# Kernel optimization log

Measured on AMD Instinct MI355X. Metric: run time of the kernel, lower is better.

Reference implementation:

```python
import jax, jax.numpy as jnp
import numpy as np

TOP_K = 8  # config['n_experts_per_token']


def setup_inputs() -> dict:
    key = jax.random.key(0)
    k1, k2 = jax.random.split(key)
    d_hidden, n_experts, n_tokens = 4096, 64, 32768
    x = jax.random.normal(k1, (n_tokens, d_hidden), dtype=jnp.float32)
    # nn.Linear weight, shape [num_experts, d_hidden], kaiming-ish scale
    W_g = jax.random.normal(k2, (n_experts, d_hidden), dtype=jnp.float32) / np.sqrt(d_hidden)
    return {"x": x, "W_g": W_g}


def reference(x, W_g):
    # logits = x @ W_g^T : [n_tokens, n_experts]
    logits = jnp.einsum('td,ed->te', x, W_g)
    scores = jax.nn.softmax(logits, axis=-1)
    # torch.topk(sorted=False) returns the same value/index set; lax.top_k is sorted
    vals, idx = jax.lax.top_k(scores, TOP_K)
    return vals, idx
```

## Files before the change

### kernel.cpp

```cpp
#include <hip/hip_runtime.h>
#include <hip/hip_fp16.h>


typedef _Float16 half8 __attribute__((ext_vector_type(8)));
typedef float floatx4 __attribute__((ext_vector_type(4)));

constexpr int D = 4096;
constexpr int NE = 64;
constexpr int MBLK = 64;
constexpr int BK = 64;
constexpr int KCHUNKS = D / BK;

__device__ __forceinline__ void split8(float4 p, float4 q, float sc, half8& h, half8& l) {
    float f[8] = {p.x, p.y, p.z, p.w, q.x, q.y, q.z, q.w};
#pragma unroll
    for (int i = 0; i < 8; ++i) {
        float v = f[i] * sc;
        _Float16 hi = (_Float16)v;
        h[i] = hi;
        l[i] = (_Float16)(v - (float)hi);
    }
}

__global__ __launch_bounds__(256, 2) void moe_gate_kernel(
    const float* __restrict__ x, const float* __restrict__ wg,
    float* __restrict__ out_vals, float* __restrict__ out_idx,
    int* __restrict__ flag_ws, int cap)
{
    __shared__ alignas(16) _Float16 Xh[MBLK * BK];
    __shared__ alignas(16) _Float16 Xl[MBLK * BK];
    __shared__ alignas(16) _Float16 Wh[NE * BK];
    __shared__ alignas(16) _Float16 Wl[NE * BK];

    const int tid  = (int)threadIdx.x;
    const int lane = tid & 63;
    const int wv   = tid >> 6;
    const int tb   = (int)blockIdx.x * MBLK;

    const int s0 = tid, s1 = tid + 256;
    const int t0 = s0 >> 3, k80 = s0 & 7;
    const int t1 = s1 >> 3, k81 = s1 & 7;

    const float* xp0 = x  + (size_t)(tb + t0) * D + k80 * 8;
    const float* xp1 = x  + (size_t)(tb + t1) * D + k81 * 8;
    const float* wp0 = wg + (size_t)t0 * D + k80 * 8;
    const float* wp1 = wg + (size_t)t1 * D + k81 * 8;

    const int xo0 = (((t0 >> 4) * 2 + (k80 >> 2)) * 64 + (k80 & 3) * 16 + (t0 & 15)) * 8;
    const int xo1 = (((t1 >> 4) * 2 + (k81 >> 2)) * 64 + (k81 & 3) * 16 + (t1 & 15)) * 8;

    float4 ra0, ra1, rb0, rb1, rc0, rc1, rd0, rd1;
#define LOADCHUNK(kc) do { const int off_ = (kc) * BK;                        \
        ra0 = *(const float4*)(xp0 + off_); ra1 = *(const float4*)(xp0 + off_ + 4); \
        rb0 = *(const float4*)(xp1 + off_); rb1 = *(const float4*)(xp1 + off_ + 4); \
        rc0 = *(const float4*)(wp0 + off_); rc1 = *(const float4*)(wp0 + off_ + 4); \
        rd0 = *(const float4*)(wp1 + off_); rd1 = *(const float4*)(wp1 + off_ + 4); } while (0)

    floatx4 acc[4] = {{0,0,0,0},{0,0,0,0},{0,0,0,0},{0,0,0,0}};

    LOADCHUNK(0);
    for (int kc = 0; kc < KCHUNKS; ++kc) {
        half8 hx0, lx0, hx1, lx1, hw0, lw0, hw1, lw1;
        split8(ra0, ra1, 1.0f,  hx0, lx0);
        split8(rb0, rb1, 1.0f,  hx1, lx1);
        split8(rc0, rc1, 64.0f, hw0, lw0);
        split8(rd0, rd1, 64.0f, hw1, lw1);
        if (kc) __syncthreads();
        *(half8*)(Xh + xo0) = hx0; *(half8*)(Xl + xo0) = lx0;
        *(half8*)(Xh + xo1) = hx1; *(half8*)(Xl + xo1) = lx1;
        *(half8*)(Wh + xo0) = hw0; *(half8*)(Wl + xo0) = lw0;
        *(half8*)(Wh + xo1) = hw1; *(half8*)(Wl + xo1) = lw1;
        if (kc + 1 < KCHUNKS) LOADCHUNK(kc + 1);
        __syncthreads();
#pragma unroll
        for (int ks = 0; ks < 2; ++ks) {
            const half8 ah = *(const half8*)(Xh + ((wv * 2 + ks) * 64 + lane) * 8);
            const half8 al = *(const half8*)(Xl + ((wv * 2 + ks) * 64 + lane) * 8);
#pragma unroll
            for (int nt = 0; nt < 4; ++nt) {
                const half8 bh = *(const half8*)(Wh + ((nt * 2 + ks) * 64 + lane) * 8);
                const half8 bl = *(const half8*)(Wl + ((nt * 2 + ks) * 64 + lane) * 8);
                acc[nt] = __builtin_amdgcn_mfma_f32_16x16x32_f16(ah, bh, acc[nt], 0, 0, 0);
                acc[nt] = __builtin_amdgcn_mfma_f32_16x16x32_f16(al, bh, acc[nt], 0, 0, 0);
                acc[nt] = __builtin_amdgcn_mfma_f32_16x16x32_f16(ah, bl, acc[nt], 0, 0, 0);
            }
        }
    }
#undef LOADCHUNK

    const int g = lane >> 4, c = lane & 15;
    const float inv64 = 0.015625f;
#pragma unroll
    for (int r = 0; r < 4; ++r) {
        float s[4];
#pragma unroll
        for (int nt = 0; nt < 4; ++nt) s[nt] = acc[nt][r] * inv64;
        float m = fmaxf(fmaxf(s[0], s[1]), fmaxf(s[2], s[3]));
#pragma unroll
        for (int off = 1; off < 16; off <<= 1) m = fmaxf(m, __shfl_xor(m, off));
        float p[4]; float t = 0.0f;
#pragma unroll
        for (int nt = 0; nt < 4; ++nt) { p[nt] = expf(s[nt] - m); t += p[nt]; }
#pragma unroll
        for (int off = 1; off < 16; off <<= 1) t += __shfl_xor(t, off);
        const float inv = 1.0f / t;
#pragma unroll
        for (int nt = 0; nt < 4; ++nt) p[nt] *= inv;

        const int tok = tb + wv * 16 + g * 4 + r;
        float prev = 0.0f;
        bool flagged = false;
#pragma unroll
        for (int i = 0; i < 9; ++i) {
            float bv = p[0]; int bn = 0;
            if (p[1] > bv) { bv = p[1]; bn = 1; }
            if (p[2] > bv) { bv = p[2]; bn = 2; }
            if (p[3] > bv) { bv = p[3]; bn = 3; }
            int be = bn * 16 + c;
#pragma unroll
            for (int off = 1; off < 16; off <<= 1) {
                float ov = __shfl_xor(bv, off);
                int   oe = __shfl_xor(be, off);
                if (ov > bv || (ov == bv && oe < be)) { bv = ov; be = oe; }
            }
            if (i > 0 && (prev - bv) < prev * 5e-5f) flagged = true;
            prev = bv;
            if (i < 8 && c == i) {
                out_vals[(size_t)tok * 8 + i] = bv;
                out_idx [(size_t)tok * 8 + i] = (float)be;
            }
            if (c == (be & 15)) p[be >> 4] = -1.0f;
        }
        if (flagged && c == 0 && cap > 0) {
            int pos = atomicAdd(flag_ws, 1);
            if (pos < cap) flag_ws[4 + pos] = tok;
        }
    }
}

__global__ __launch_bounds__(256) void moe_refine_kernel(
    const float* __restrict__ x, const float* __restrict__ wg,
    float* __restrict__ out_vals, float* __restrict__ out_idx,
    const int* __restrict__ flag_ws, int cap)
{
    const int count = min(flag_ws[0], cap);
    const int* list = flag_ws + 4;
    __shared__ double part[256];
    for (int it = (int)blockIdx.x; it < count; it += (int)gridDim.x) {
        const int tok = list[it];
        const int e = (int)threadIdx.x & 63, ch = (int)threadIdx.x >> 6;
        const float4* xr = (const float4*)(x + (size_t)tok * D + ch * 1024);
        const float4* wr = (const float4*)(wg + (size_t)e * D + ch * 1024);
        double s0 = 0, s1 = 0, s2 = 0, s3 = 0;
#pragma unroll 4
        for (int k = 0; k < 256; ++k) {
            float4 a = xr[k], b = wr[k];
            s0 += (double)a.x * (double)b.x; s1 += (double)a.y * (double)b.y;
            s2 += (double)a.z * (double)b.z; s3 += (double)a.w * (double)b.w;
        }
        part[threadIdx.x] = (s0 + s1) + (s2 + s3);
        __syncthreads();
        if (threadIdx.x < 64) {
            double l = part[e] + part[e + 64] + part[e + 128] + part[e + 192];
            double m = l;
#pragma unroll
            for (int off = 1; off < 64; off <<= 1) m = fmax(m, __shfl_xor(m, off));
            double p = exp(l - m), Z = p;
#pragma unroll
            for (int off = 1; off < 64; off <<= 1) Z += __shfl_xor(Z, off);
            double key = l;
            for (int i = 0; i < 8; ++i) {
                double bk = key; int bi = e; double bp = p;
#pragma unroll
                for (int off = 1; off < 64; off <<= 1) {
                    double ok = __shfl_xor(bk, off);
                    int    oi = __shfl_xor(bi, off);
                    double op = __shfl_xor(bp, off);
                    if (ok > bk || (ok == bk && oi < bi)) { bk = ok; bi = oi; bp = op; }
                }
                if (e == i) {
                    out_vals[(size_t)tok * 8 + i] = (float)(bp / Z);
                    out_idx [(size_t)tok * 8 + i] = (float)bi;
                }
                if (e == bi) key = -1.0e300;
            }
        }
        __syncthreads();
    }
}

extern "C" void kernel_launch(void* const* d_in, const int* in_sizes, int n_in,
                              void* d_out, int out_size, void* d_ws, size_t ws_size,
                              hipStream_t stream) {
    const float* x  = (const float*)d_in[0];
    const float* wg = (const float*)d_in[1];
    const int n_tokens = in_sizes[0] / D;
    float* out_vals = (float*)d_out;
    float* out_idx  = out_vals + (size_t)n_tokens * 8;
    int cap = 0;
    if (ws_size > 32) {
        size_t c = (ws_size - 32) / sizeof(int);
        cap = (int)(c > 32768 ? 32768 : c);
    }
    hipMemsetAsync(d_ws, 0, 16, stream);
    const int grid = n_tokens / MBLK;
    hipLaunchKernelGGL(moe_gate_kernel, dim3(grid), dim3(256), 0, stream,
                       x, wg, out_vals, out_idx, (int*)d_ws, cap);
    hipLaunchKernelGGL(moe_refine_kernel, dim3(256), dim3(256), 0, stream,
                       x, wg, out_vals, out_idx, (const int*)d_ws, cap);
}
```

Measured before the change: 795.0 us.

## Prepack gate weights to fp16 hi/lo and stream X directly into registers

Adds a small pre-kernel that splits W_g into fp16 hi/lo parts once per call, in the MFMA-friendly tiled layout, and stores them in the workspace. The gate kernel then pulls each W chunk into double-buffered LDS with global_load_lds async copies. Each wave loads its X rows straight into registers in the MFMA A-operand layout, so X no longer goes through LDS. This removes the per-block repeated W conversion, the X LDS round trip, and one barrier per chunk. In exchange it adds an extra launch and needs more workspace, since the packed weights sit at a fixed 256KB offset.

```diff
diff --git a/kernel.cpp b/kernel.cpp
--- a/kernel.cpp
+++ b/kernel.cpp
@@ -11,7 +11,10 @@
 constexpr int BK = 64;
 constexpr int KCHUNKS = D / BK;
 
-__device__ __forceinline__ void split8(float4 p, float4 q, float sc, half8& h, half8& l) {
+constexpr size_t WPACK_OFF  = 1u << 18;
+constexpr size_t WPACK_HALF = (size_t)KCHUNKS * NE * BK;
+
+__device__ __forceinline__ void split8s(float4 p, float4 q, float sc, half8& h, half8& l) {
     float f[8] = {p.x, p.y, p.z, p.w, q.x, q.y, q.z, q.w};
 #pragma unroll
     for (int i = 0; i < 8; ++i) {
@@ -22,71 +25,110 @@
     }
 }
 
+__device__ __forceinline__ void async16(const _Float16* g, _Float16* lds) {
+    __builtin_amdgcn_global_load_lds(
+        (__attribute__((address_space(1))) uint32_t*)g,
+        (__attribute__((address_space(3))) uint32_t*)lds, 16, 0, 0);
+}
+
+__global__ __launch_bounds__(256) void moe_pack_w(
+    const float* __restrict__ wg, _Float16* __restrict__ whp, _Float16* __restrict__ wlp)
+{
+    const int kc = (int)blockIdx.x;
+    const int tid = (int)threadIdx.x;
+#pragma unroll
+    for (int r = 0; r < 2; ++r) {
+        const int s = tid + r * 256;
+        const int e = s >> 3, k8 = s & 7;
+        const float* src = wg + (size_t)e * D + kc * BK + k8 * 8;
+        float4 a = *(const float4*)src;
+        float4 b = *(const float4*)(src + 4);
+        half8 h, l;
+        split8s(a, b, 64.0f, h, l);
+        const int off = (((e >> 4) * 2 + (k8 >> 2)) * 64 + (k8 & 3) * 16 + (e & 15)) * 8;
+        *(half8*)(whp + (size_t)kc * 4096 + off) = h;
+        *(half8*)(wlp + (size_t)kc * 4096 + off) = l;
+    }
+}
+
 __global__ __launch_bounds__(256, 2) void moe_gate_kernel(
-    const float* __restrict__ x, const float* __restrict__ wg,
+    const float* __restrict__ x,
+    const _Float16* __restrict__ whp, const _Float16* __restrict__ wlp,
     float* __restrict__ out_vals, float* __restrict__ out_idx,
     int* __restrict__ flag_ws, int cap)
 {
-    __shared__ alignas(16) _Float16 Xh[MBLK * BK];
-    __shared__ alignas(16) _Float16 Xl[MBLK * BK];
-    __shared__ alignas(16) _Float16 Wh[NE * BK];
-    __shared__ alignas(16) _Float16 Wl[NE * BK];
+    __shared__ alignas(16) _Float16 WhB[2 * NE * BK];
+    __shared__ alignas(16) _Float16 WlB[2 * NE * BK];
 
     const int tid  = (int)threadIdx.x;
     const int lane = tid & 63;
     const int wv   = tid >> 6;
     const int tb   = (int)blockIdx.x * MBLK;
 
-    const int s0 = tid, s1 = tid + 256;
-    const int t0 = s0 >> 3, k80 = s0 & 7;
-    const int t1 = s1 >> 3, k81 = s1 & 7;
-
-    const float* xp0 = x  + (size_t)(tb + t0) * D + k80 * 8;
-    const float* xp1 = x  + (size_t)(tb + t1) * D + k81 * 8;
-    const float* wp0 = wg + (size_t)t0 * D + k80 * 8;
-    const float* wp1 = wg + (size_t)t1 * D + k81 * 8;
-
-    const int xo0 = (((t0 >> 4) * 2 + (k80 >> 2)) * 64 + (k80 & 3) * 16 + (t0 & 15)) * 8;
-    const int xo1 = (((t1 >> 4) * 2 + (k81 >> 2)) * 64 + (k81 & 3) * 16 + (t1 & 15)) * 8;
-
-    float4 ra0, ra1, rb0, rb1, rc0, rc1, rd0, rd1;
-#define LOADCHUNK(kc) do { const int off_ = (kc) * BK;                        \
-        ra0 = *(const float4*)(xp0 + off_); ra1 = *(const float4*)(xp0 + off_ + 4); \
-        rb0 = *(const float4*)(xp1 + off_); rb1 = *(const float4*)(xp1 + off_ + 4); \
-        rc0 = *(const float4*)(wp0 + off_); rc1 = *(const float4*)(wp0 + off_ + 4); \
-        rd0 = *(const float4*)(wp1 + off_); rd1 = *(const float4*)(wp1 + off_ + 4); } while (0)
+    const float* xp = x + (size_t)(tb + wv * 16 + (lane & 15)) * D + (lane >> 4) * 8;
+
+    const int wgo = wv * 1024 + lane * 8;
+    const int wlo = wv * 1024;
 
     floatx4 acc[4] = {{0,0,0,0},{0,0,0,0},{0,0,0,0},{0,0,0,0}};
 
-    LOADCHUNK(0);
-    for (int kc = 0; kc < KCHUNKS; ++kc) {
-        half8 hx0, lx0, hx1, lx1, hw0, lw0, hw1, lw1;
-        split8(ra0, ra1, 1.0f,  hx0, lx0);
-        split8(rb0, rb1, 1.0f,  hx1, lx1);
-        split8(rc0, rc1, 64.0f, hw0, lw0);
-        split8(rd0, rd1, 64.0f, hw1, lw1);
-        if (kc) __syncthreads();
-        *(half8*)(Xh + xo0) = hx0; *(half8*)(Xl + xo0) = lx0;
-        *(half8*)(Xh + xo1) = hx1; *(half8*)(Xl + xo1) = lx1;
-        *(half8*)(Wh + xo0) = hw0; *(half8*)(Wl + xo0) = lw0;
-        *(half8*)(Wh + xo1) = hw1; *(half8*)(Wl + xo1) = lw1;
-        if (kc + 1 < KCHUNKS) LOADCHUNK(kc + 1);
+    async16(whp + wgo,       WhB + wlo);
+    async16(whp + wgo + 512, WhB + wlo + 512);
+    async16(wlp + wgo,       WlB + wlo);
+    async16(wlp + wgo + 512, WlB + wlo + 512);
+    float4 A0 = *(const float4*)(xp);
+    float4 A1 = *(const float4*)(xp + 4);
+    float4 A2 = *(const float4*)(xp + 32);
+    float4 A3 = *(const float4*)(xp + 36);
+    float4 B0, B1, B2, B3;
+    asm volatile("s_waitcnt vmcnt(0)" ::: "memory");
+    __syncthreads();
+
+    auto body = [&](int kc, float4& C0, float4& C1, float4& C2, float4& C3,
+                    float4& N0, float4& N1, float4& N2, float4& N3) {
+        if (kc + 1 < KCHUNKS) {
+            const int nb = (kc + 1) & 1;
+            const _Float16* gh = whp + (size_t)(kc + 1) * 4096 + wgo;
+            const _Float16* gl = wlp + (size_t)(kc + 1) * 4096 + wgo;
+            async16(gh,       WhB + nb * 4096 + wlo);
+            async16(gh + 512, WhB + nb * 4096 + wlo + 512);
+            async16(gl,       WlB + nb * 4096 + wlo);
+            async16(gl + 512, WlB + nb * 4096 + wlo + 512);
+            const float* xn = xp + (kc + 1) * 64;
+            N0 = *(const float4*)(xn);
+            N1 = *(const float4*)(xn + 4);
+            N2 = *(const float4*)(xn + 32);
+            N3 = *(const float4*)(xn + 36);
+        }
+        half8 ah0, al0, ah1, al1;
+        split8s(C0, C1, 1.0f, ah0, al0);
+        split8s(C2, C3, 1.0f, ah1, al1);
+        const _Float16* wh = WhB + (kc & 1) * 4096;
+        const _Float16* wl = WlB + (kc & 1) * 4096;
+#pragma unroll
+        for (int nt = 0; nt < 4; ++nt) {
+            const half8 bh = *(const half8*)(wh + ((nt * 2 + 0) * 64 + lane) * 8);
+            const half8 bl = *(const half8*)(wl + ((nt * 2 + 0) * 64 + lane) * 8);
+            acc[nt] = __builtin_amdgcn_mfma_f32_16x16x32_f16(ah0, bh, acc[nt], 0, 0, 0);
+            acc[nt] = __builtin_amdgcn_mfma_f32_16x16x32_f16(al0, bh, acc[nt], 0, 0, 0);
+            acc[nt] = __builtin_amdgcn_mfma_f32_16x16x32_f16(ah0, bl, acc[nt], 0, 0, 0);
+        }
+#pragma unroll
+        for (int nt = 0; nt < 4; ++nt) {
+            const half8 bh = *(const half8*)(wh + ((nt * 2 + 1) * 64 + lane) * 8);
+            const half8 bl = *(const half8*)(wl + ((nt * 2 + 1) * 64 + lane) * 8);
+            acc[nt] = __builtin_amdgcn_mfma_f32_16x16x32_f16(ah1, bh, acc[nt], 0, 0, 0);
+            acc[nt] = __builtin_amdgcn_mfma_f32_16x16x32_f16(al1, bh, acc[nt], 0, 0, 0);
+            acc[nt] = __builtin_amdgcn_mfma_f32_16x16x32_f16(ah1, bl, acc[nt], 0, 0, 0);
+        }
+        asm volatile("s_waitcnt vmcnt(0)" ::: "memory");
         __syncthreads();
-#pragma unroll
-        for (int ks = 0; ks < 2; ++ks) {
-            const half8 ah = *(const half8*)(Xh + ((wv * 2 + ks) * 64 + lane) * 8);
-            const half8 al = *(const half8*)(Xl + ((wv * 2 + ks) * 64 + lane) * 8);
-#pragma unroll
-            for (int nt = 0; nt < 4; ++nt) {
-                const half8 bh = *(const half8*)(Wh + ((nt * 2 + ks) * 64 + lane) * 8);
-                const half8 bl = *(const half8*)(Wl + ((nt * 2 + ks) * 64 + lane) * 8);
-                acc[nt] = __builtin_amdgcn_mfma_f32_16x16x32_f16(ah, bh, acc[nt], 0, 0, 0);
-                acc[nt] = __builtin_amdgcn_mfma_f32_16x16x32_f16(al, bh, acc[nt], 0, 0, 0);
-                acc[nt] = __builtin_amdgcn_mfma_f32_16x16x32_f16(ah, bl, acc[nt], 0, 0, 0);
-            }
-        }
-    }
-#undef LOADCHUNK
+    };
+
+    for (int kc = 0; kc < KCHUNKS; kc += 2) {
+        body(kc,     A0, A1, A2, A3, B0, B1, B2, B3);
+        body(kc + 1, B0, B1, B2, B3, A0, A1, A2, A3);
+    }
 
     const int g = lane >> 4, c = lane & 15;
     const float inv64 = 0.015625f;
@@ -197,15 +239,18 @@
     const int n_tokens = in_sizes[0] / D;
     float* out_vals = (float*)d_out;
     float* out_idx  = out_vals + (size_t)n_tokens * 8;
+    _Float16* whp = (_Float16*)((char*)d_ws + WPACK_OFF);
+    _Float16* wlp = whp + WPACK_HALF;
     int cap = 0;
     if (ws_size > 32) {
         size_t c = (ws_size - 32) / sizeof(int);
         cap = (int)(c > 32768 ? 32768 : c);
     }
     hipMemsetAsync(d_ws, 0, 16, stream);
+    hipLaunchKernelGGL(moe_pack_w, dim3(KCHUNKS), dim3(256), 0, stream, wg, whp, wlp);
     const int grid = n_tokens / MBLK;
     hipLaunchKernelGGL(moe_gate_kernel, dim3(grid), dim3(256), 0, stream,
-                       x, wg, out_vals, out_idx, (int*)d_ws, cap);
+                       x, whp, wlp, out_vals, out_idx, (int*)d_ws, cap);
     hipLaunchKernelGGL(moe_refine_kernel, dim3(256), dim3(256), 0, stream,
                        x, wg, out_vals, out_idx, (const int*)d_ws, cap);
 }
```

New measurement: 787.0 us. No clear change (-1.0%).
